# Kernel optimization log

Measured on AMD Instinct MI355X. Metric: run time of the kernel, lower is better.

Reference implementation:

```python
import jax, jax.numpy as jnp
import numpy as np

B, T, DIM = 4, 2048, 1024
H, DH = 16, 64  # num_heads, dim_head = dim // num_heads


def setup_inputs() -> dict:
    key = jax.random.key(0)
    k1, k2, k3 = jax.random.split(key, 3)
    x = jax.random.normal(k1, (B, T, DIM), dtype=jnp.float32)
    # nn.Linear weights stored as [out_features, in_features]
    w_qkv = jax.random.normal(k2, (3 * H * DH, DIM), dtype=jnp.float32) * (DIM ** -0.5)
    w_out = jax.random.normal(k3, (DIM, H * DH), dtype=jnp.float32) * ((H * DH) ** -0.5)
    b_out = jnp.zeros((DIM,), dtype=jnp.float32)
    return {"x": x, "w_qkv": w_qkv, "w_out": w_out, "b_out": b_out}


def reference(x, w_qkv, w_out, b_out):
    b, t, dim = x.shape
    # qkv projection (Linear, no bias): [b, t, 3*H*DH]
    qkv = jnp.einsum('btd,ed->bte', x, w_qkv)
    # einops 'b t (d k h) -> k b h t d' with k=3, h=H: dim_head outermost, heads innermost
    qkv = qkv.reshape(b, t, DH, 3, H)            # [b, t, d, k, h]
    qkv = jnp.transpose(qkv, (3, 0, 4, 1, 2))    # [k, b, h, t, d]
    q, k_, v = qkv[0], qkv[1], qkv[2]
    scale = dim ** -0.5  # note: scales by dim, not dim_head (faithful to source)
    attn = jnp.einsum('bhid,bhjd->bhij', q, k_) * scale
    attn = jax.nn.softmax(attn, axis=-1)
    out = jnp.einsum('bhij,bhjd->bhid', attn, v)  # [b, h, t, d]
    # 'b h t d -> b t (h d)'
    out = jnp.transpose(out, (0, 2, 1, 3)).reshape(b, t, H * DH)
    return jnp.einsum('bte,de->btd', out, w_out) + b_out
```

## Files before the change

kernel.cpp:

```cpp
#include <hip/hip_runtime.h>
#include <stdint.h>

typedef unsigned short ushort_t;
typedef __attribute__((ext_vector_type(8))) short short8;
typedef __attribute__((ext_vector_type(4))) short short4v;
typedef __attribute__((ext_vector_type(4))) float f32x4;
typedef __attribute__((ext_vector_type(16))) float f32x16;

#define B_ 4
#define T_ 2048
#define H_ 16
#define DH_ 64
#define DIM_ 1024
#define NE_ 3072
#define LOG2E 1.4426950408889634f

__device__ __forceinline__ ushort_t f2bf(float f) {
  union { float f; uint32_t u; } v; v.f = f;
  uint32_t u = v.u;
  uint32_t r = (u + 0x7FFFu + ((u >> 16) & 1u)) >> 16;
  return (ushort_t)r;
}
__device__ __forceinline__ void gload16(const void* g, void* l) {
  __builtin_amdgcn_global_load_lds(
      (__attribute__((address_space(1))) void*)g,
      (__attribute__((address_space(3))) void*)l, 16, 0, 0);
}
__device__ __forceinline__ uint32_t cvtpk(float a, float b) {
  uint32_t r;
  asm("v_cvt_pk_bf16_f32 %0, %1, %2" : "=v"(r) : "v"(a), "v"(b));
  return r;
}
__device__ __forceinline__ float exp2_asm(float x) {
  float r; asm("v_exp_f32 %0, %1" : "=v"(r) : "v"(x)); return r;
}
__device__ __forceinline__ float max3f(float a, float b, float c) {
  float d; asm("v_max3_f32 %0, %1, %2, %3" : "=v"(d) : "v"(a), "v"(b), "v"(c));
  return d;
}

__global__ __launch_bounds__(256)
void cvt_f32_bf16(const float* __restrict__ in, ushort_t* __restrict__ out, long n) {
  const long i = ((long)blockIdx.x * 256 + threadIdx.x) * 4;
  if (i >= n) return;
  const float4 v = *(const float4*)(in + i);
  short4v o;
  o[0] = (short)f2bf(v.x); o[1] = (short)f2bf(v.y);
  o[2] = (short)f2bf(v.z); o[3] = (short)f2bf(v.w);
  *(short4v*)(out + i) = o;
}

template<int MODE>
__global__ __launch_bounds__(256)
void gemm_bt(const ushort_t* __restrict__ A, const ushort_t* __restrict__ Bm,
             ushort_t* __restrict__ Cb, float* __restrict__ Cf,
             const float* __restrict__ bias, int M, int N, int K, int nb) {
  __shared__ __align__(16) ushort_t Alds[128 * 32];
  __shared__ __align__(16) ushort_t Blds[128 * 32];
  const int tid = threadIdx.x;
  const int wave = tid >> 6, lane = tid & 63;
  const int bid = blockIdx.x;
  const int bm0 = (bid / nb) << 7, bn0 = (bid % nb) << 7;
  const int l4 = lane >> 4, l15 = lane & 15;
  const int srow = lane >> 2;
  const int scol = (lane & 3) * 8;
  const int wr = (wave >> 1) * 64, wc = (wave & 1) * 64;

  f32x4 acc[4][4];
#pragma unroll
  for (int i = 0; i < 4; ++i)
#pragma unroll
    for (int j = 0; j < 4; ++j) acc[i][j] = {0.f, 0.f, 0.f, 0.f};

  for (int k0 = 0; k0 < K; k0 += 32) {
    __syncthreads();
#pragma unroll
    for (int c = 0; c < 2; ++c) {
      const int r0 = wave * 32 + c * 16;
      gload16(A + (long)(bm0 + r0 + srow) * K + k0 + scol, Alds + r0 * 32);
      gload16(Bm + (long)(bn0 + r0 + srow) * K + k0 + scol, Blds + r0 * 32);
    }
    __syncthreads();
    short8 af[4], bfr[4];
#pragma unroll
    for (int i = 0; i < 4; ++i)
      af[i] = *(const short8*)(Alds + (wr + i * 16 + l15) * 32 + l4 * 8);
#pragma unroll
    for (int j = 0; j < 4; ++j)
      bfr[j] = *(const short8*)(Blds + (wc + j * 16 + l15) * 32 + l4 * 8);
#pragma unroll
    for (int i = 0; i < 4; ++i)
#pragma unroll
      for (int j = 0; j < 4; ++j)
        acc[i][j] = __builtin_amdgcn_mfma_f32_16x16x32_bf16(af[i], bfr[j], acc[i][j], 0, 0, 0);
  }

#pragma unroll
  for (int i = 0; i < 4; ++i) {
    const int row = bm0 + wr + i * 16 + l4 * 4;
#pragma unroll
    for (int j = 0; j < 4; ++j) {
      const int col = bn0 + wc + j * 16 + l15;
      if (MODE == 0) {
        const float mult = (((col >> 4) % 3) == 0) ? 0.04508422f : 1.f;
#pragma unroll
        for (int r = 0; r < 4; ++r)
          Cb[(long)(row + r) * N + col] = f2bf(acc[i][j][r] * mult);
      } else {
        const float add = bias[col];
#pragma unroll
        for (int r = 0; r < 4; ++r)
          Cf[(long)(row + r) * N + col] = acc[i][j][r] + add;
      }
    }
  }
}

__global__ __launch_bounds__(256)
void reorg(const ushort_t* __restrict__ qkv, ushort_t* __restrict__ Qh,
           ushort_t* __restrict__ Kh, ushort_t* __restrict__ Vth) {
  __shared__ __align__(16) ushort_t lds[8 * 3080];
  const int bid = blockIdx.x;
  const int tt = bid & 255, b = bid >> 8;
  const int t0 = tt * 8;
  const int tid = threadIdx.x;
  const short8* src = (const short8*)(qkv + ((long)(b * T_ + t0)) * NE_);
  short8* dst = (short8*)lds;
  for (int i = tid; i < 8 * 384; i += 256) {
    const int r = i / 384, c = i - r * 384;
    dst[r * 385 + c] = src[i];
  }
  __syncthreads();
  for (int i = tid; i < 16 * 8 * 8; i += 256) {
    const int dblk = i & 7, t = (i >> 3) & 7, h = i >> 6;
    short8 vq, vk;
#pragma unroll
    for (int e = 0; e < 8; ++e) {
      const int d = dblk * 8 + e;
      vq[e] = (short)lds[t * 3080 + d * 48 + h];
      vk[e] = (short)lds[t * 3080 + d * 48 + 16 + h];
    }
    const long o = ((long)((b * H_ + h) * T_) + t0 + t) * DH_ + dblk * 8;
    *(short8*)(Qh + o) = vq;
    *(short8*)(Kh + o) = vk;
  }
  for (int i = tid; i < 16 * 64; i += 256) {
    const int d = i & 63, h = i >> 6;
    short8 v0;
#pragma unroll
    for (int t = 0; t < 8; ++t) v0[t] = (short)lds[t * 3080 + d * 48 + 32 + h];
    const long o = ((long)((b * H_ + h) * DH_) + d) * T_ + t0;
    *(short8*)(Vth + o) = v0;
  }
}

#define MFMA32(a, b, c) __builtin_amdgcn_mfma_f32_32x32x16_bf16(a, b, c, 0, 0, 0)

__global__ __launch_bounds__(256, 4)
void attn_fwd3(const ushort_t* __restrict__ Qh, const ushort_t* __restrict__ Kh,
               const ushort_t* __restrict__ Vth, ushort_t* __restrict__ aout) {
  __shared__ __align__(16) ushort_t Kt[64 * 64];
  __shared__ __align__(16) ushort_t Vts[64 * 64];
  const int bid = blockIdx.x;
  const int xcd = bid & 7, idx = bid >> 3;
  const int bh = xcd + ((idx & 7) << 3);
  const int qb = idx >> 3;
  const int tid = threadIdx.x, wv = tid >> 6, lane = tid & 63;
  const int l31 = lane & 31, hi = lane >> 5, l7 = lane & 7, l8 = lane >> 3;
  const ushort_t* Qb = Qh + (long)bh * T_ * DH_;
  const ushort_t* Kb = Kh + (long)bh * T_ * DH_;
  const ushort_t* Vb = Vth + (long)bh * DH_ * T_;
  const int q = qb * 128 + wv * 32 + l31;

  short8 qf[4];
#pragma unroll
  for (int s = 0; s < 4; ++s)
    qf[s] = *(const short8*)(Qb + (long)q * DH_ + s * 16 + hi * 8);

  f32x16 acc0, acc1;
#pragma unroll
  for (int i = 0; i < 16; ++i) { acc0[i] = 0.f; acc1[i] = 0.f; }
  float mhat = 0.f, lsum = 0.f;

  const int r0a = wv * 16;
  const int sl = ((l7 ^ l8) * 8);

  for (int j0 = 0; j0 < T_; j0 += 64) {
    __syncthreads();
#pragma unroll
    for (int c = 0; c < 2; ++c) {
      const int rr = r0a + c * 8 + l8;
      gload16(Kb + (long)(j0 + rr) * DH_ + sl, Kt + (r0a + c * 8) * 64);
      gload16(Vb + (long)rr * T_ + j0 + sl, Vts + (r0a + c * 8) * 64);
    }
    __syncthreads();

    const float negm = -mhat;
    f32x16 sb0, sb1;
#pragma unroll
    for (int i = 0; i < 16; ++i) { sb0[i] = negm; sb1[i] = negm; }
    __builtin_amdgcn_s_setprio(1);
#pragma unroll
    for (int s = 0; s < 4; ++s) {
      const int so = ((2 * s + hi) ^ l7) * 8;
      const short8 k0 = *(const short8*)(Kt + (l31) * 64 + so);
      const short8 k1 = *(const short8*)(Kt + (32 + l31) * 64 + so);
      sb0 = MFMA32(k0, qf[s], sb0);
      sb1 = MFMA32(k1, qf[s], sb1);
    }
    __builtin_amdgcn_s_setprio(0);

    float t0 = max3f(sb0[0], sb0[1], sb0[2]);
    float t1 = max3f(sb0[3], sb0[4], sb0[5]);
    float t2 = max3f(sb0[6], sb0[7], sb0[8]);
    float t3 = max3f(sb0[9], sb0[10], sb0[11]);
    float t4 = max3f(sb0[12], sb0[13], sb0[14]);
    float t5 = max3f(sb1[0], sb1[1], sb1[2]);
    float t6 = max3f(sb1[3], sb1[4], sb1[5]);
    float t7 = max3f(sb1[6], sb1[7], sb1[8]);
    float t8 = max3f(sb1[9], sb1[10], sb1[11]);
    float t9 = max3f(sb1[12], sb1[13], sb1[14]);
    float ta = fmaxf(sb0[15], sb1[15]);
    float u0 = max3f(t0, t1, t2);
    float u1 = max3f(t3, t4, t5);
    float u2 = max3f(t6, t7, t8);
    float u3 = max3f(t9, ta, u0);
    float pmax = max3f(u1, u2, u3);
    pmax = fmaxf(pmax, __shfl_xor(pmax, 32));

    if (!__all(pmax <= 8.f)) {
      const float delta = fmaxf(pmax, 0.f);
      const float corr = exp2_asm(-delta);
      lsum *= corr;
#pragma unroll
      for (int i = 0; i < 16; ++i) {
        acc0[i] *= corr; acc1[i] *= corr;
        sb0[i] -= delta; sb1[i] -= delta;
      }
      mhat += delta;
    }

    float r0 = 0.f, r1 = 0.f, r2 = 0.f, r3 = 0.f;
#pragma unroll
    for (int i = 0; i < 16; i += 4) {
      sb0[i]     = exp2_asm(sb0[i]);     r0 += sb0[i];
      sb0[i + 1] = exp2_asm(sb0[i + 1]); r1 += sb0[i + 1];
      sb0[i + 2] = exp2_asm(sb0[i + 2]); r2 += sb0[i + 2];
      sb0[i + 3] = exp2_asm(sb0[i + 3]); r3 += sb0[i + 3];
    }
#pragma unroll
    for (int i = 0; i < 16; i += 4) {
      sb1[i]     = exp2_asm(sb1[i]);     r0 += sb1[i];
      sb1[i + 1] = exp2_asm(sb1[i + 1]); r1 += sb1[i + 1];
      sb1[i + 2] = exp2_asm(sb1[i + 2]); r2 += sb1[i + 2];
      sb1[i + 3] = exp2_asm(sb1[i + 3]); r3 += sb1[i + 3];
    }
    float rs = (r0 + r1) + (r2 + r3);
    lsum += rs + __shfl_xor(rs, 32);

    short8 pf[4];
#pragma unroll
    for (int ks = 0; ks < 4; ++ks) {
      const f32x16& S = (ks < 2) ? sb0 : sb1;
      const int rb = (ks & 1) * 8;
      uint32_t wE0 = cvtpk(S[rb + 0], S[rb + 1]);
      uint32_t wE1 = cvtpk(S[rb + 2], S[rb + 3]);
      uint32_t wO0 = cvtpk(S[rb + 4], S[rb + 5]);
      uint32_t wO1 = cvtpk(S[rb + 6], S[rb + 7]);
      asm("v_permlane32_swap_b32 %0, %1" : "+v"(wE0), "+v"(wO0));
      asm("v_permlane32_swap_b32 %0, %1" : "+v"(wE1), "+v"(wO1));
      union { uint32_t u[4]; short8 v; } pk;
      pk.u[0] = wE0; pk.u[1] = wE1; pk.u[2] = wO0; pk.u[3] = wO1;
      pf[ks] = pk.v;
    }

    __builtin_amdgcn_s_setprio(1);
#pragma unroll
    for (int ks = 0; ks < 4; ++ks) {
      const int so = ((2 * ks + hi) ^ l7) * 8;
      const short8 v0 = *(const short8*)(Vts + (l31) * 64 + so);
      const short8 v1 = *(const short8*)(Vts + (32 + l31) * 64 + so);
      acc0 = MFMA32(v0, pf[ks], acc0);
      acc1 = MFMA32(v1, pf[ks], acc1);
    }
    __builtin_amdgcn_s_setprio(0);
  }

  const float inv = 1.f / lsum;
  const int b = bh >> 4, h = bh & 15;
  ushort_t* orow = aout + ((long)(b * T_ + q)) * DIM_ + h * DH_;
#pragma unroll
  for (int vb = 0; vb < 2; ++vb)
#pragma unroll
    for (int rg = 0; rg < 4; ++rg) {
      short4v o4;
#pragma unroll
      for (int e = 0; e < 4; ++e) {
        const float val = ((vb == 0) ? acc0[rg * 4 + e] : acc1[rg * 4 + e]) * inv;
        o4[e] = (short)f2bf(val);
      }
      *(short4v*)(orow + vb * 32 + rg * 8 + hi * 4) = o4;
    }
}

extern "C" void kernel_launch(void* const* d_in, const int* in_sizes, int n_in,
                              void* d_out, int out_size, void* d_ws, size_t ws_size,
                              hipStream_t stream) {
  const float* x_f    = (const float*)d_in[0];
  const float* wqkv_f = (const float*)d_in[1];
  const float* wout_f = (const float*)d_in[2];
  const float* bout_f = (const float*)d_in[3];
  float* out = (float*)d_out;

  ushort_t* wqkv_bf = (ushort_t*)d_ws;
  ushort_t* wout_bf = wqkv_bf + (long)NE_ * DIM_;
  ushort_t* qkv     = wout_bf + (long)DIM_ * DIM_;
  ushort_t* R       = qkv + (long)B_ * T_ * NE_;
  ushort_t* x_bf = R;
  ushort_t* Qh   = R;
  ushort_t* Kh   = R + (long)B_ * H_ * T_ * DH_;
  ushort_t* Vth  = Kh + (long)B_ * H_ * T_ * DH_;
  ushort_t* aout = qkv;

  cvt_f32_bf16<<<dim3(8192), dim3(256), 0, stream>>>(x_f, x_bf, (long)B_ * T_ * DIM_);
  cvt_f32_bf16<<<dim3(3072), dim3(256), 0, stream>>>(wqkv_f, wqkv_bf, (long)NE_ * DIM_);
  cvt_f32_bf16<<<dim3(1024), dim3(256), 0, stream>>>(wout_f, wout_bf, (long)DIM_ * DIM_);

  gemm_bt<0><<<dim3((8192 / 128) * (3072 / 128)), dim3(256), 0, stream>>>(
      x_bf, wqkv_bf, qkv, nullptr, nullptr, 8192, 3072, 1024, 3072 / 128);
  reorg<<<dim3(1024), dim3(256), 0, stream>>>(qkv, Qh, Kh, Vth);
  attn_fwd3<<<dim3(1024), dim3(256), 0, stream>>>(Qh, Kh, Vth, aout);
  gemm_bt<1><<<dim3((8192 / 128) * (1024 / 128)), dim3(256), 0, stream>>>(
      aout, wout_bf, nullptr, out, bout_f, 8192, 1024, 1024, 1024 / 128);
}
```

Before: 233.1 us.

## Process 64 queries per wave and double-buffer K/V tiles in attention

Each attention wave now handles two 32-row query tiles, so every K and V fragment read from LDS feeds twice as many MFMAs. The grid is halved to 512 blocks. K/V tiles are double-buffered in LDS, with the next tile's global-to-LDS load issued before computing the current one, and an explicit vmcnt wait plus barrier replaces the two syncthreads. The cost is much higher register use, with launch bounds dropped to 2 blocks, and fewer blocks to spread across the CUs. The softmax max is also shared across both query tiles, which could raise the rescale frequency.

```diff
diff --git a/kernel.cpp b/kernel.cpp
--- a/kernel.cpp
+++ b/kernel.cpp
@@ -37,6 +37,24 @@
 __device__ __forceinline__ float max3f(float a, float b, float c) {
   float d; asm("v_max3_f32 %0, %1, %2, %3" : "=v"(d) : "v"(a), "v"(b), "v"(c));
   return d;
+}
+__device__ __forceinline__ float tile_max(const f32x16& a, const f32x16& b) {
+  float t0 = max3f(a[0], a[1], a[2]);
+  float t1 = max3f(a[3], a[4], a[5]);
+  float t2 = max3f(a[6], a[7], a[8]);
+  float t3 = max3f(a[9], a[10], a[11]);
+  float t4 = max3f(a[12], a[13], a[14]);
+  float t5 = max3f(b[0], b[1], b[2]);
+  float t6 = max3f(b[3], b[4], b[5]);
+  float t7 = max3f(b[6], b[7], b[8]);
+  float t8 = max3f(b[9], b[10], b[11]);
+  float t9 = max3f(b[12], b[13], b[14]);
+  float ta = fmaxf(a[15], b[15]);
+  float u0 = max3f(t0, t1, t2);
+  float u1 = max3f(t3, t4, t5);
+  float u2 = max3f(t6, t7, t8);
+  float u3 = max3f(t9, ta, u0);
+  return max3f(u1, u2, u3);
 }
 
 __global__ __launch_bounds__(256)
@@ -156,150 +174,190 @@
 
 #define MFMA32(a, b, c) __builtin_amdgcn_mfma_f32_32x32x16_bf16(a, b, c, 0, 0, 0)
 
-__global__ __launch_bounds__(256, 4)
-void attn_fwd3(const ushort_t* __restrict__ Qh, const ushort_t* __restrict__ Kh,
+__global__ __launch_bounds__(256, 2)
+void attn_fwd4(const ushort_t* __restrict__ Qh, const ushort_t* __restrict__ Kh,
                const ushort_t* __restrict__ Vth, ushort_t* __restrict__ aout) {
-  __shared__ __align__(16) ushort_t Kt[64 * 64];
-  __shared__ __align__(16) ushort_t Vts[64 * 64];
+  __shared__ __align__(16) ushort_t Kt[2][64 * 64];
+  __shared__ __align__(16) ushort_t Vts[2][64 * 64];
   const int bid = blockIdx.x;
   const int xcd = bid & 7, idx = bid >> 3;
   const int bh = xcd + ((idx & 7) << 3);
-  const int qb = idx >> 3;
+  const int qsb = idx >> 3;
   const int tid = threadIdx.x, wv = tid >> 6, lane = tid & 63;
   const int l31 = lane & 31, hi = lane >> 5, l7 = lane & 7, l8 = lane >> 3;
   const ushort_t* Qb = Qh + (long)bh * T_ * DH_;
   const ushort_t* Kb = Kh + (long)bh * T_ * DH_;
   const ushort_t* Vb = Vth + (long)bh * DH_ * T_;
-  const int q = qb * 128 + wv * 32 + l31;
-
-  short8 qf[4];
-#pragma unroll
-  for (int s = 0; s < 4; ++s)
-    qf[s] = *(const short8*)(Qb + (long)q * DH_ + s * 16 + hi * 8);
-
-  f32x16 acc0, acc1;
-#pragma unroll
-  for (int i = 0; i < 16; ++i) { acc0[i] = 0.f; acc1[i] = 0.f; }
-  float mhat = 0.f, lsum = 0.f;
+  const int q0 = qsb * 256 + wv * 64;
+
+  short8 qfA[4], qfB[4];
+#pragma unroll
+  for (int s = 0; s < 4; ++s) {
+    qfA[s] = *(const short8*)(Qb + (long)(q0 + l31) * DH_ + s * 16 + hi * 8);
+    qfB[s] = *(const short8*)(Qb + (long)(q0 + 32 + l31) * DH_ + s * 16 + hi * 8);
+  }
+
+  f32x16 accA0, accA1, accB0, accB1;
+#pragma unroll
+  for (int i = 0; i < 16; ++i) {
+    accA0[i] = 0.f; accA1[i] = 0.f; accB0[i] = 0.f; accB1[i] = 0.f;
+  }
+  float mhat = 0.f, lsumA = 0.f, lsumB = 0.f;
 
   const int r0a = wv * 16;
   const int sl = ((l7 ^ l8) * 8);
 
+#define STAGE(bufi, jj)                                                        \
+  do {                                                                         \
+    _Pragma("unroll")                                                          \
+    for (int c = 0; c < 2; ++c) {                                              \
+      const int rr = r0a + c * 8 + l8;                                         \
+      gload16(Kb + (long)((jj) + rr) * DH_ + sl, &Kt[bufi][(r0a + c * 8) * 64]); \
+      gload16(Vb + (long)rr * T_ + (jj) + sl, &Vts[bufi][(r0a + c * 8) * 64]); \
+    }                                                                          \
+  } while (0)
+
+  STAGE(0, 0);
+  int buf = 0;
+
   for (int j0 = 0; j0 < T_; j0 += 64) {
-    __syncthreads();
-#pragma unroll
-    for (int c = 0; c < 2; ++c) {
-      const int rr = r0a + c * 8 + l8;
-      gload16(Kb + (long)(j0 + rr) * DH_ + sl, Kt + (r0a + c * 8) * 64);
-      gload16(Vb + (long)rr * T_ + j0 + sl, Vts + (r0a + c * 8) * 64);
-    }
-    __syncthreads();
-
+    STAGE(buf ^ 1, (j0 + 64) & (T_ - 1));
+    asm volatile("s_waitcnt vmcnt(4)" ::: "memory");
+    __builtin_amdgcn_sched_barrier(0);
+    __builtin_amdgcn_s_barrier();
+
+    const ushort_t* Ktb = &Kt[buf][0];
+    const ushort_t* Vtb = &Vts[buf][0];
     const float negm = -mhat;
-    f32x16 sb0, sb1;
-#pragma unroll
-    for (int i = 0; i < 16; ++i) { sb0[i] = negm; sb1[i] = negm; }
+
+    f32x16 sA0, sA1, sB0, sB1;
+#pragma unroll
+    for (int i = 0; i < 16; ++i) { sA0[i] = negm; sA1[i] = negm; sB0[i] = negm; sB1[i] = negm; }
     __builtin_amdgcn_s_setprio(1);
 #pragma unroll
     for (int s = 0; s < 4; ++s) {
       const int so = ((2 * s + hi) ^ l7) * 8;
-      const short8 k0 = *(const short8*)(Kt + (l31) * 64 + so);
-      const short8 k1 = *(const short8*)(Kt + (32 + l31) * 64 + so);
-      sb0 = MFMA32(k0, qf[s], sb0);
-      sb1 = MFMA32(k1, qf[s], sb1);
+      const short8 k0 = *(const short8*)(Ktb + (l31) * 64 + so);
+      const short8 k1 = *(const short8*)(Ktb + (32 + l31) * 64 + so);
+      sA0 = MFMA32(k0, qfA[s], sA0);
+      sA1 = MFMA32(k1, qfA[s], sA1);
+      sB0 = MFMA32(k0, qfB[s], sB0);
+      sB1 = MFMA32(k1, qfB[s], sB1);
     }
     __builtin_amdgcn_s_setprio(0);
 
-    float t0 = max3f(sb0[0], sb0[1], sb0[2]);
-    float t1 = max3f(sb0[3], sb0[4], sb0[5]);
-    float t2 = max3f(sb0[6], sb0[7], sb0[8]);
-    float t3 = max3f(sb0[9], sb0[10], sb0[11]);
-    float t4 = max3f(sb0[12], sb0[13], sb0[14]);
-    float t5 = max3f(sb1[0], sb1[1], sb1[2]);
-    float t6 = max3f(sb1[3], sb1[4], sb1[5]);
-    float t7 = max3f(sb1[6], sb1[7], sb1[8]);
-    float t8 = max3f(sb1[9], sb1[10], sb1[11]);
-    float t9 = max3f(sb1[12], sb1[13], sb1[14]);
-    float ta = fmaxf(sb0[15], sb1[15]);
-    float u0 = max3f(t0, t1, t2);
-    float u1 = max3f(t3, t4, t5);
-    float u2 = max3f(t6, t7, t8);
-    float u3 = max3f(t9, ta, u0);
-    float pmax = max3f(u1, u2, u3);
+    float pmax = fmaxf(tile_max(sA0, sA1), tile_max(sB0, sB1));
     pmax = fmaxf(pmax, __shfl_xor(pmax, 32));
-
     if (!__all(pmax <= 8.f)) {
       const float delta = fmaxf(pmax, 0.f);
       const float corr = exp2_asm(-delta);
-      lsum *= corr;
+      lsumA *= corr; lsumB *= corr;
 #pragma unroll
       for (int i = 0; i < 16; ++i) {
-        acc0[i] *= corr; acc1[i] *= corr;
-        sb0[i] -= delta; sb1[i] -= delta;
+        accA0[i] *= corr; accA1[i] *= corr; accB0[i] *= corr; accB1[i] *= corr;
+        sA0[i] -= delta; sA1[i] -= delta; sB0[i] -= delta; sB1[i] -= delta;
       }
       mhat += delta;
     }
 
-    float r0 = 0.f, r1 = 0.f, r2 = 0.f, r3 = 0.f;
-#pragma unroll
-    for (int i = 0; i < 16; i += 4) {
-      sb0[i]     = exp2_asm(sb0[i]);     r0 += sb0[i];
-      sb0[i + 1] = exp2_asm(sb0[i + 1]); r1 += sb0[i + 1];
-      sb0[i + 2] = exp2_asm(sb0[i + 2]); r2 += sb0[i + 2];
-      sb0[i + 3] = exp2_asm(sb0[i + 3]); r3 += sb0[i + 3];
-    }
-#pragma unroll
-    for (int i = 0; i < 16; i += 4) {
-      sb1[i]     = exp2_asm(sb1[i]);     r0 += sb1[i];
-      sb1[i + 1] = exp2_asm(sb1[i + 1]); r1 += sb1[i + 1];
-      sb1[i + 2] = exp2_asm(sb1[i + 2]); r2 += sb1[i + 2];
-      sb1[i + 3] = exp2_asm(sb1[i + 3]); r3 += sb1[i + 3];
-    }
-    float rs = (r0 + r1) + (r2 + r3);
-    lsum += rs + __shfl_xor(rs, 32);
-
-    short8 pf[4];
-#pragma unroll
-    for (int ks = 0; ks < 4; ++ks) {
-      const f32x16& S = (ks < 2) ? sb0 : sb1;
-      const int rb = (ks & 1) * 8;
-      uint32_t wE0 = cvtpk(S[rb + 0], S[rb + 1]);
-      uint32_t wE1 = cvtpk(S[rb + 2], S[rb + 3]);
-      uint32_t wO0 = cvtpk(S[rb + 4], S[rb + 5]);
-      uint32_t wO1 = cvtpk(S[rb + 6], S[rb + 7]);
-      asm("v_permlane32_swap_b32 %0, %1" : "+v"(wE0), "+v"(wO0));
-      asm("v_permlane32_swap_b32 %0, %1" : "+v"(wE1), "+v"(wO1));
-      union { uint32_t u[4]; short8 v; } pk;
-      pk.u[0] = wE0; pk.u[1] = wE1; pk.u[2] = wO0; pk.u[3] = wO1;
-      pf[ks] = pk.v;
-    }
+    {
+      float r0 = 0.f, r1 = 0.f, r2 = 0.f, r3 = 0.f;
+#pragma unroll
+      for (int i = 0; i < 16; i += 4) {
+        sA0[i]     = exp2_asm(sA0[i]);     r0 += sA0[i];
+        sA0[i + 1] = exp2_asm(sA0[i + 1]); r1 += sA0[i + 1];
+        sA0[i + 2] = exp2_asm(sA0[i + 2]); r2 += sA0[i + 2];
+        sA0[i + 3] = exp2_asm(sA0[i + 3]); r3 += sA0[i + 3];
+      }
+#pragma unroll
+      for (int i = 0; i < 16; i += 4) {
+        sA1[i]     = exp2_asm(sA1[i]);     r0 += sA1[i];
+        sA1[i + 1] = exp2_asm(sA1[i + 1]); r1 += sA1[i + 1];
+        sA1[i + 2] = exp2_asm(sA1[i + 2]); r2 += sA1[i + 2];
+        sA1[i + 3] = exp2_asm(sA1[i + 3]); r3 += sA1[i + 3];
+      }
+      float rs = (r0 + r1) + (r2 + r3);
+      lsumA += rs + __shfl_xor(rs, 32);
+    }
+    {
+      float r0 = 0.f, r1 = 0.f, r2 = 0.f, r3 = 0.f;
+#pragma unroll
+      for (int i = 0; i < 16; i += 4) {
+        sB0[i]     = exp2_asm(sB0[i]);     r0 += sB0[i];
+        sB0[i + 1] = exp2_asm(sB0[i + 1]); r1 += sB0[i + 1];
+        sB0[i + 2] = exp2_asm(sB0[i + 2]); r2 += sB0[i + 2];
+        sB0[i + 3] = exp2_asm(sB0[i + 3]); r3 += sB0[i + 3];
+      }
+#pragma unroll
+      for (int i = 0; i < 16; i += 4) {
+        sB1[i]     = exp2_asm(sB1[i]);     r0 += sB1[i];
+        sB1[i + 1] = exp2_asm(sB1[i + 1]); r1 += sB1[i + 1];
+        sB1[i + 2] = exp2_asm(sB1[i + 2]); r2 += sB1[i + 2];
+        sB1[i + 3] = exp2_asm(sB1[i + 3]); r3 += sB1[i + 3];
+      }
+      float rs = (r0 + r1) + (r2 + r3);
+      lsumB += rs + __shfl_xor(rs, 32);
+    }
+
+#define PF_BUILD(pf, S0, S1)                                                   \
+  do {                                                                         \
+    _Pragma("unroll")                                                          \
+    for (int ks = 0; ks < 4; ++ks) {                                           \
+      const f32x16& S = (ks < 2) ? (S0) : (S1);                                \
+      const int rb = (ks & 1) * 8;                                             \
+      uint32_t wE0 = cvtpk(S[rb + 0], S[rb + 1]);                              \
+      uint32_t wE1 = cvtpk(S[rb + 2], S[rb + 3]);                              \
+      uint32_t wO0 = cvtpk(S[rb + 4], S[rb + 5]);                              \
+      uint32_t wO1 = cvtpk(S[rb + 6], S[rb + 7]);                              \
+      asm("v_permlane32_swap_b32 %0, %1" : "+v"(wE0), "+v"(wO0));              \
+      asm("v_permlane32_swap_b32 %0, %1" : "+v"(wE1), "+v"(wO1));              \
+      union { uint32_t u[4]; short8 v; } pk;                                   \
+      pk.u[0] = wE0; pk.u[1] = wE1; pk.u[2] = wO0; pk.u[3] = wO1;              \
+      pf[ks] = pk.v;                                                           \
+    }                                                                          \
+  } while (0)
+
+    short8 pfA[4];
+    PF_BUILD(pfA, sA0, sA1);
+    short8 pfB[4];
+    PF_BUILD(pfB, sB0, sB1);
 
     __builtin_amdgcn_s_setprio(1);
 #pragma unroll
     for (int ks = 0; ks < 4; ++ks) {
       const int so = ((2 * ks + hi) ^ l7) * 8;
-      const short8 v0 = *(const short8*)(Vts + (l31) * 64 + so);
-      const short8 v1 = *(const short8*)(Vts + (32 + l31) * 64 + so);
-      acc0 = MFMA32(v0, pf[ks], acc0);
-      acc1 = MFMA32(v1, pf[ks], acc1);
+      const short8 v0 = *(const short8*)(Vtb + (l31) * 64 + so);
+      const short8 v1 = *(const short8*)(Vtb + (32 + l31) * 64 + so);
+      accA0 = MFMA32(v0, pfA[ks], accA0);
+      accA1 = MFMA32(v1, pfA[ks], accA1);
+      accB0 = MFMA32(v0, pfB[ks], accB0);
+      accB1 = MFMA32(v1, pfB[ks], accB1);
     }
     __builtin_amdgcn_s_setprio(0);
-  }
-
-  const float inv = 1.f / lsum;
+
+    __builtin_amdgcn_sched_barrier(0);
+    __builtin_amdgcn_s_barrier();
+    buf ^= 1;
+  }
+
   const int b = bh >> 4, h = bh & 15;
-  ushort_t* orow = aout + ((long)(b * T_ + q)) * DIM_ + h * DH_;
+  const float invA = 1.f / lsumA, invB = 1.f / lsumB;
+  ushort_t* orowA = aout + ((long)(b * T_ + q0 + l31)) * DIM_ + h * DH_;
+  ushort_t* orowB = aout + ((long)(b * T_ + q0 + 32 + l31)) * DIM_ + h * DH_;
 #pragma unroll
   for (int vb = 0; vb < 2; ++vb)
 #pragma unroll
     for (int rg = 0; rg < 4; ++rg) {
-      short4v o4;
+      short4v oA, oB;
 #pragma unroll
       for (int e = 0; e < 4; ++e) {
-        const float val = ((vb == 0) ? acc0[rg * 4 + e] : acc1[rg * 4 + e]) * inv;
-        o4[e] = (short)f2bf(val);
-      }
-      *(short4v*)(orow + vb * 32 + rg * 8 + hi * 4) = o4;
+        const float vA = ((vb == 0) ? accA0[rg * 4 + e] : accA1[rg * 4 + e]) * invA;
+        const float vB = ((vb == 0) ? accB0[rg * 4 + e] : accB1[rg * 4 + e]) * invB;
+        oA[e] = (short)f2bf(vA);
+        oB[e] = (short)f2bf(vB);
+      }
+      *(short4v*)(orowA + vb * 32 + rg * 8 + hi * 4) = oA;
+      *(short4v*)(orowB + vb * 32 + rg * 8 + hi * 4) = oB;
     }
 }
 
@@ -329,7 +387,7 @@
   gemm_bt<0><<<dim3((8192 / 128) * (3072 / 128)), dim3(256), 0, stream>>>(
       x_bf, wqkv_bf, qkv, nullptr, nullptr, 8192, 3072, 1024, 3072 / 128);
   reorg<<<dim3(1024), dim3(256), 0, stream>>>(qkv, Qh, Kh, Vth);
-  attn_fwd3<<<dim3(1024), dim3(256), 0, stream>>>(Qh, Kh, Vth, aout);
+  attn_fwd4<<<dim3(512), dim3(256), 0, stream>>>(Qh, Kh, Vth, aout);
   gemm_bt<1><<<dim3((8192 / 128) * (1024 / 128)), dim3(256), 0, stream>>>(
       aout, wout_bf, nullptr, out, bout_f, 8192, 1024, 1024, 1024 / 128);
 }
```

New measurement: 229.4 us. Within noise of the previous version (-1.6%).

## Double-buffer K/V tiles in attention and XCD-remap GEMM block order

Applied to the files above, without the earlier changes.

The attention kernel now keeps two LDS buffers for K and V and issues the global-to-LDS loads for the next 64-key tile before computing on the current one, so load latency overlaps with MFMA and softmax work. This replaces two barriers per iteration with one wait-and-barrier at the end. Separately, the GEMM remaps block IDs so that consecutive tiles land on the same XCD, which should improve L2 reuse. The double buffer doubles attention LDS to 32KB per block, which could reduce occupancy at 4 blocks per CU. On the last iteration the kernel also does a redundant wrap-around prefetch.

```diff
diff --git a/kernel.cpp b/kernel.cpp
--- a/kernel.cpp
+++ b/kernel.cpp
@@ -37,6 +37,24 @@
 __device__ __forceinline__ float max3f(float a, float b, float c) {
   float d; asm("v_max3_f32 %0, %1, %2, %3" : "=v"(d) : "v"(a), "v"(b), "v"(c));
   return d;
+}
+__device__ __forceinline__ float tile_max(const f32x16& a, const f32x16& b) {
+  float t0 = max3f(a[0], a[1], a[2]);
+  float t1 = max3f(a[3], a[4], a[5]);
+  float t2 = max3f(a[6], a[7], a[8]);
+  float t3 = max3f(a[9], a[10], a[11]);
+  float t4 = max3f(a[12], a[13], a[14]);
+  float t5 = max3f(b[0], b[1], b[2]);
+  float t6 = max3f(b[3], b[4], b[5]);
+  float t7 = max3f(b[6], b[7], b[8]);
+  float t8 = max3f(b[9], b[10], b[11]);
+  float t9 = max3f(b[12], b[13], b[14]);
+  float ta = fmaxf(a[15], b[15]);
+  float u0 = max3f(t0, t1, t2);
+  float u1 = max3f(t3, t4, t5);
+  float u2 = max3f(t6, t7, t8);
+  float u3 = max3f(t9, ta, u0);
+  return max3f(u1, u2, u3);
 }
 
 __global__ __launch_bounds__(256)
@@ -59,7 +77,8 @@
   __shared__ __align__(16) ushort_t Blds[128 * 32];
   const int tid = threadIdx.x;
   const int wave = tid >> 6, lane = tid & 63;
-  const int bid = blockIdx.x;
+  const int cpx = gridDim.x >> 3;
+  const int bid = (blockIdx.x & 7) * cpx + (blockIdx.x >> 3);
   const int bm0 = (bid / nb) << 7, bn0 = (bid % nb) << 7;
   const int l4 = lane >> 4, l15 = lane & 15;
   const int srow = lane >> 2;
@@ -157,10 +176,10 @@
 #define MFMA32(a, b, c) __builtin_amdgcn_mfma_f32_32x32x16_bf16(a, b, c, 0, 0, 0)
 
 __global__ __launch_bounds__(256, 4)
-void attn_fwd3(const ushort_t* __restrict__ Qh, const ushort_t* __restrict__ Kh,
+void attn_fwd5(const ushort_t* __restrict__ Qh, const ushort_t* __restrict__ Kh,
                const ushort_t* __restrict__ Vth, ushort_t* __restrict__ aout) {
-  __shared__ __align__(16) ushort_t Kt[64 * 64];
-  __shared__ __align__(16) ushort_t Vts[64 * 64];
+  __shared__ __align__(16) ushort_t Kt[2][64 * 64];
+  __shared__ __align__(16) ushort_t Vts[2][64 * 64];
   const int bid = blockIdx.x;
   const int xcd = bid & 7, idx = bid >> 3;
   const int bh = xcd + ((idx & 7) << 3);
@@ -185,17 +204,30 @@
   const int r0a = wv * 16;
   const int sl = ((l7 ^ l8) * 8);
 
+#define STAGE(bufi, jj)                                                          \
+  do {                                                                           \
+    _Pragma("unroll")                                                            \
+    for (int c = 0; c < 2; ++c) {                                                \
+      const int rr = r0a + c * 8 + l8;                                           \
+      gload16(Kb + (long)((jj) + rr) * DH_ + sl, &Kt[bufi][(r0a + c * 8) * 64]); \
+      gload16(Vb + (long)rr * T_ + (jj) + sl, &Vts[bufi][(r0a + c * 8) * 64]);   \
+    }                                                                            \
+  } while (0)
+
+  STAGE(0, 0);
+  asm volatile("s_waitcnt vmcnt(0)" ::: "memory");
+  __builtin_amdgcn_sched_barrier(0);
+  __builtin_amdgcn_s_barrier();
+  __builtin_amdgcn_sched_barrier(0);
+
+  int buf = 0;
   for (int j0 = 0; j0 < T_; j0 += 64) {
-    __syncthreads();
-#pragma unroll
-    for (int c = 0; c < 2; ++c) {
-      const int rr = r0a + c * 8 + l8;
-      gload16(Kb + (long)(j0 + rr) * DH_ + sl, Kt + (r0a + c * 8) * 64);
-      gload16(Vb + (long)rr * T_ + j0 + sl, Vts + (r0a + c * 8) * 64);
-    }
-    __syncthreads();
-
+    STAGE(buf ^ 1, (j0 + 64) & (T_ - 1));
+
+    const ushort_t* Ktb = &Kt[buf][0];
+    const ushort_t* Vtb = &Vts[buf][0];
     const float negm = -mhat;
+
     f32x16 sb0, sb1;
 #pragma unroll
     for (int i = 0; i < 16; ++i) { sb0[i] = negm; sb1[i] = negm; }
@@ -203,31 +235,15 @@
 #pragma unroll
     for (int s = 0; s < 4; ++s) {
       const int so = ((2 * s + hi) ^ l7) * 8;
-      const short8 k0 = *(const short8*)(Kt + (l31) * 64 + so);
-      const short8 k1 = *(const short8*)(Kt + (32 + l31) * 64 + so);
+      const short8 k0 = *(const short8*)(Ktb + (l31) * 64 + so);
+      const short8 k1 = *(const short8*)(Ktb + (32 + l31) * 64 + so);
       sb0 = MFMA32(k0, qf[s], sb0);
       sb1 = MFMA32(k1, qf[s], sb1);
     }
     __builtin_amdgcn_s_setprio(0);
 
-    float t0 = max3f(sb0[0], sb0[1], sb0[2]);
-    float t1 = max3f(sb0[3], sb0[4], sb0[5]);
-    float t2 = max3f(sb0[6], sb0[7], sb0[8]);
-    float t3 = max3f(sb0[9], sb0[10], sb0[11]);
-    float t4 = max3f(sb0[12], sb0[13], sb0[14]);
-    float t5 = max3f(sb1[0], sb1[1], sb1[2]);
-    float t6 = max3f(sb1[3], sb1[4], sb1[5]);
-    float t7 = max3f(sb1[6], sb1[7], sb1[8]);
-    float t8 = max3f(sb1[9], sb1[10], sb1[11]);
-    float t9 = max3f(sb1[12], sb1[13], sb1[14]);
-    float ta = fmaxf(sb0[15], sb1[15]);
-    float u0 = max3f(t0, t1, t2);
-    float u1 = max3f(t3, t4, t5);
-    float u2 = max3f(t6, t7, t8);
-    float u3 = max3f(t9, ta, u0);
-    float pmax = max3f(u1, u2, u3);
+    float pmax = tile_max(sb0, sb1);
     pmax = fmaxf(pmax, __shfl_xor(pmax, 32));
-
     if (!__all(pmax <= 8.f)) {
       const float delta = fmaxf(pmax, 0.f);
       const float corr = exp2_asm(-delta);
@@ -278,12 +294,18 @@
 #pragma unroll
     for (int ks = 0; ks < 4; ++ks) {
       const int so = ((2 * ks + hi) ^ l7) * 8;
-      const short8 v0 = *(const short8*)(Vts + (l31) * 64 + so);
-      const short8 v1 = *(const short8*)(Vts + (32 + l31) * 64 + so);
+      const short8 v0 = *(const short8*)(Vtb + (l31) * 64 + so);
+      const short8 v1 = *(const short8*)(Vtb + (32 + l31) * 64 + so);
       acc0 = MFMA32(v0, pf[ks], acc0);
       acc1 = MFMA32(v1, pf[ks], acc1);
     }
     __builtin_amdgcn_s_setprio(0);
+
+    asm volatile("s_waitcnt vmcnt(0)" ::: "memory");
+    __builtin_amdgcn_sched_barrier(0);
+    __builtin_amdgcn_s_barrier();
+    __builtin_amdgcn_sched_barrier(0);
+    buf ^= 1;
   }
 
   const float inv = 1.f / lsum;
@@ -329,7 +351,7 @@
   gemm_bt<0><<<dim3((8192 / 128) * (3072 / 128)), dim3(256), 0, stream>>>(
       x_bf, wqkv_bf, qkv, nullptr, nullptr, 8192, 3072, 1024, 3072 / 128);
   reorg<<<dim3(1024), dim3(256), 0, stream>>>(qkv, Qh, Kh, Vth);
-  attn_fwd3<<<dim3(1024), dim3(256), 0, stream>>>(Qh, Kh, Vth, aout);
+  attn_fwd5<<<dim3(1024), dim3(256), 0, stream>>>(Qh, Kh, Vth, aout);
   gemm_bt<1><<<dim3((8192 / 128) * (1024 / 128)), dim3(256), 0, stream>>>(
       aout, wout_bf, nullptr, out, bout_f, 8192, 1024, 1024, 1024 / 128);
 }
```

New measurement: 233.0 us. No clear change (-0.0%).
